# Optimization experiments

Measured on AMD Instinct MI355X. Metric: run time of the kernel, lower is better.

Reference implementation:

```python
import jax, jax.numpy as jnp
import numpy as np
import math

TAU = 1.0  # init kwarg tau


def setup_inputs() -> dict:
    key = jax.random.key(0)
    n, m = 1024, 8192
    V = jax.random.normal(key, (n, m), dtype=jnp.float32)
    return {"V": V}


def reference(V) -> jnp.ndarray:
    n, m = V.shape
    num_rounds = math.ceil(m / n)
    # Repeat V row-blocks num_rounds times: M has shape [num_rounds*n, m]
    M = jnp.tile(V, (num_rounds, 1))

    def step(c, row):
        # Soft round-robin pick (training branch of SoftRR.__one_round)
        y = jax.nn.softmax((row - jnp.min(row) + 1.0) * c / TAU)
        c = (1.0 - y) * c
        return c, y

    c0 = jnp.ones((m,), dtype=V.dtype)
    _, R = jax.lax.scan(step, c0, M)  # R: [num_rounds*n, m]
    pi = R.reshape(num_rounds, n, m).sum(axis=0)  # [n, m]
    return pi
```

## Files before the change

kernel.cpp:

```cpp
#include <hip/hip_runtime.h>
#include <hip/hip_fp16.h>


#define N_ROWS 1024
#define M_COLS 8192
#define STEPS  8192
#define LOG2E  1.4426950408889634f

using half8  = __attribute__((ext_vector_type(8))) _Float16;
using half2v = __attribute__((ext_vector_type(2))) _Float16;

__device__ __forceinline__ float fast_exp2(float x) {
#if __has_builtin(__builtin_amdgcn_exp2f)
  return __builtin_amdgcn_exp2f(x);
#else
  return exp2f(x);
#endif
}
__device__ __forceinline__ float fast_rcp(float x) {
#if __has_builtin(__builtin_amdgcn_rcpf)
  return __builtin_amdgcn_rcpf(x);
#else
  return 1.0f / x;
#endif
}
__device__ __forceinline__ half2v pack_f16(float y0, float y1) {
  return __builtin_bit_cast(half2v, __builtin_amdgcn_cvt_pkrtz(y0, y1));
}

template <int CTRL>
__device__ __forceinline__ float dpp_add(float x) {
  int yi = __builtin_amdgcn_update_dpp(0, __builtin_bit_cast(int, x),
                                       CTRL, 0xf, 0xf, true);
  return x + __builtin_bit_cast(float, yi);
}

__device__ __forceinline__ float wave_sum_to_lane63(float x) {
  x = dpp_add<0x111>(x);
  x = dpp_add<0x112>(x);
  x = dpp_add<0x114>(x);
  x = dpp_add<0x118>(x);
  x = dpp_add<0x142>(x);
  x = dpp_add<0x143>(x);
  return x;
}

#define BAR_LDS_ONLY() asm volatile("s_waitcnt lgkmcnt(0)\n\ts_barrier" ::: "memory")

__global__ void softrr_rowmin(const float* __restrict__ V, float* __restrict__ rmin) {
  const int row = blockIdx.x;
  const float* p = V + (size_t)row * M_COLS;
  float m = 1e30f;
  for (int j = threadIdx.x; j < M_COLS; j += 256) m = fminf(m, p[j]);
#pragma unroll
  for (int off = 32; off; off >>= 1) m = fminf(m, __shfl_xor(m, off, 64));
  __shared__ float sm[4];
  if ((threadIdx.x & 63) == 0) sm[threadIdx.x >> 6] = m;
  __syncthreads();
  if (threadIdx.x == 0) {
    rmin[row] = fminf(fminf(sm[0], sm[1]), fminf(sm[2], sm[3]));
  }
}

__global__ void softrr_prep(const float* __restrict__ V, const float* __restrict__ rmin,
                            __half* __restrict__ A) {
  const int idx8 = blockIdx.x * 256 + threadIdx.x;
  const int row = idx8 >> 10;
  const float mn = rmin[row];
  const float4* v4 = (const float4*)V;
  float4 va = v4[2 * idx8];
  float4 vb = v4[2 * idx8 + 1];
  half8 o;
  o[0] = (_Float16)((va.x - mn + 1.0f) * LOG2E);
  o[1] = (_Float16)((va.y - mn + 1.0f) * LOG2E);
  o[2] = (_Float16)((va.z - mn + 1.0f) * LOG2E);
  o[3] = (_Float16)((va.w - mn + 1.0f) * LOG2E);
  o[4] = (_Float16)((vb.x - mn + 1.0f) * LOG2E);
  o[5] = (_Float16)((vb.y - mn + 1.0f) * LOG2E);
  o[6] = (_Float16)((vb.z - mn + 1.0f) * LOG2E);
  o[7] = (_Float16)((vb.w - mn + 1.0f) * LOG2E);
  ((half8*)A)[idx8] = o;
}

__global__ void __launch_bounds__(512) softrr_scan_nor(const __half* __restrict__ Ah,
                                                       __half* __restrict__ Rh) {
  const int t = threadIdx.x;
  const int wave = t >> 6;
  const int lane = t & 63;
  __shared__ float sP[2][8];

  const half8* __restrict__ A8 = (const half8*)Ah;
  half8* __restrict__ R8 = (half8*)Rh;

  float c[16];
#pragma unroll
  for (int k = 0; k < 16; ++k) c[k] = 1.0f;

  half8 a_cur0 = A8[2 * t];
  half8 a_cur1 = A8[2 * t + 1];
  half8 a_nx0  = A8[1024 + 2 * t];
  half8 a_nx1  = A8[1024 + 2 * t + 1];

  for (int s = 0; s < STEPS; ++s) {
    const int ld  = (s + 2) & (N_ROWS - 1);
    const int par = s & 1;

    half8 an0 = A8[ld * 1024 + 2 * t];
    half8 an1 = A8[ld * 1024 + 2 * t + 1];

    float e[16];
#pragma unroll
    for (int k = 0; k < 8; ++k) {
      e[k]     = fast_exp2((float)a_cur0[k] * c[k]);
      e[8 + k] = fast_exp2((float)a_cur1[k] * c[8 + k]);
    }
    float l = (((e[0] + e[1]) + (e[2] + e[3])) + ((e[4] + e[5]) + (e[6] + e[7])))
            + (((e[8] + e[9]) + (e[10] + e[11])) + ((e[12] + e[13]) + (e[14] + e[15])));

    l = wave_sum_to_lane63(l);
    if (lane == 63) sP[par][wave] = l;
    BAR_LDS_ONLY();

    float x = (lane < 8) ? sP[par][lane] : 0.0f;
    x = dpp_add<0x111>(x);
    x = dpp_add<0x112>(x);
    x = dpp_add<0x114>(x);
    const float S = __builtin_bit_cast(
        float, __builtin_amdgcn_readlane(__builtin_bit_cast(int, x), 7));
    const float Sinv = fast_rcp(S);

    half8 o0, o1;
#pragma unroll
    for (int k = 0; k < 8; k += 2) {
      float y0 = e[k] * Sinv;
      float y1 = e[k + 1] * Sinv;
      c[k]     = __builtin_fmaf(-y0, c[k], c[k]);
      c[k + 1] = __builtin_fmaf(-y1, c[k + 1], c[k + 1]);
      half2v h = pack_f16(y0, y1);
      o0[k] = h[0]; o0[k + 1] = h[1];
    }
#pragma unroll
    for (int k = 0; k < 8; k += 2) {
      float y0 = e[8 + k] * Sinv;
      float y1 = e[8 + k + 1] * Sinv;
      c[8 + k]     = __builtin_fmaf(-y0, c[8 + k], c[8 + k]);
      c[8 + k + 1] = __builtin_fmaf(-y1, c[8 + k + 1], c[8 + k + 1]);
      half2v h = pack_f16(y0, y1);
      o1[k] = h[0]; o1[k + 1] = h[1];
    }
    R8[(size_t)s * 1024 + 2 * t]     = o0;
    R8[(size_t)s * 1024 + 2 * t + 1] = o1;

    a_cur0 = a_nx0; a_cur1 = a_nx1;
    a_nx0 = an0;    a_nx1 = an1;
  }
}

__global__ void softrr_sum8(const __half* __restrict__ Rh, float* __restrict__ out) {
  const int idx8 = blockIdx.x * 256 + threadIdx.x;
  const half8* R8 = (const half8*)Rh;
  float acc[8];
  {
    half8 v = R8[idx8];
#pragma unroll
    for (int k = 0; k < 8; ++k) acc[k] = (float)v[k];
  }
#pragma unroll
  for (int r = 1; r < 8; ++r) {
    half8 v = R8[(size_t)r * 1024 * 1024 + idx8];
#pragma unroll
    for (int k = 0; k < 8; ++k) acc[k] += (float)v[k];
  }
  ((float4*)out)[2 * idx8]     = make_float4(acc[0], acc[1], acc[2], acc[3]);
  ((float4*)out)[2 * idx8 + 1] = make_float4(acc[4], acc[5], acc[6], acc[7]);
}

__global__ void __launch_bounds__(512) softrr_scan_a(const __half* __restrict__ Ah,
                                                     __half* __restrict__ PIh) {
  const int t = threadIdx.x;
  const int wave = t >> 6;
  const int lane = t & 63;
  __shared__ float sP[2][8];
  const half8* __restrict__ A8 = (const half8*)Ah;
  half8* __restrict__ P8 = (half8*)PIh;
  float c[16];
#pragma unroll
  for (int k = 0; k < 16; ++k) c[k] = 1.0f;
  half8 a0 = A8[2 * t];
  half8 a1 = A8[2 * t + 1];
  half8 p0, p1;
  for (int s = 0; s < STEPS; ++s) {
    const int i = s & (N_ROWS - 1);
    const int r = s >> 10;
    const int in_ = (s + 1) & (N_ROWS - 1);
    const int par = s & 1;
    half8 an0 = A8[in_ * 1024 + 2 * t];
    half8 an1 = A8[in_ * 1024 + 2 * t + 1];
    float e[16];
#pragma unroll
    for (int k = 0; k < 8; ++k) {
      e[k]     = fast_exp2((float)a0[k] * c[k]);
      e[8 + k] = fast_exp2((float)a1[k] * c[8 + k]);
    }
    float l = (((e[0] + e[1]) + (e[2] + e[3])) + ((e[4] + e[5]) + (e[6] + e[7])))
            + (((e[8] + e[9]) + (e[10] + e[11])) + ((e[12] + e[13]) + (e[14] + e[15])));
    l = wave_sum_to_lane63(l);
    if (lane == 63) sP[par][wave] = l;
    BAR_LDS_ONLY();
    float x = (lane < 8) ? sP[par][lane] : 0.0f;
    x = dpp_add<0x111>(x);
    x = dpp_add<0x112>(x);
    x = dpp_add<0x114>(x);
    const float S = __builtin_bit_cast(
        float, __builtin_amdgcn_readlane(__builtin_bit_cast(int, x), 7));
    const float Sinv = fast_rcp(S);
    half8 o0, o1;
#pragma unroll
    for (int k = 0; k < 8; k += 2) {
      float y0 = e[k] * Sinv, y1 = e[k + 1] * Sinv;
      c[k] = __builtin_fmaf(-y0, c[k], c[k]);
      c[k + 1] = __builtin_fmaf(-y1, c[k + 1], c[k + 1]);
      half2v h = pack_f16(y0, y1);
      o0[k] = h[0]; o0[k + 1] = h[1];
    }
#pragma unroll
    for (int k = 0; k < 8; k += 2) {
      float y0 = e[8 + k] * Sinv, y1 = e[8 + k + 1] * Sinv;
      c[8 + k] = __builtin_fmaf(-y0, c[8 + k], c[8 + k]);
      c[8 + k + 1] = __builtin_fmaf(-y1, c[8 + k + 1], c[8 + k + 1]);
      half2v h = pack_f16(y0, y1);
      o1[k] = h[0]; o1[k + 1] = h[1];
    }
    if (r > 0) { o0 = o0 + p0; o1 = o1 + p1; }
    P8[i * 1024 + 2 * t]     = o0;
    P8[i * 1024 + 2 * t + 1] = o1;
    a0 = an0; a1 = an1;
    p0 = P8[in_ * 1024 + 2 * t];
    p1 = P8[in_ * 1024 + 2 * t + 1];
  }
}

__global__ void softrr_cvt(const __half* __restrict__ PIh, float* __restrict__ out) {
  const int idx8 = blockIdx.x * 256 + threadIdx.x;
  half8 p = ((const half8*)PIh)[idx8];
  ((float4*)out)[2 * idx8]     = make_float4((float)p[0], (float)p[1], (float)p[2], (float)p[3]);
  ((float4*)out)[2 * idx8 + 1] = make_float4((float)p[4], (float)p[5], (float)p[6], (float)p[7]);
}

__global__ void __launch_bounds__(1024) softrr_scan_b(const float* __restrict__ V,
                                                      const float* __restrict__ rmin,
                                                      float* __restrict__ out) {
  const int t = threadIdx.x;
  const int wave = t >> 6;
  const int lane = t & 63;
  __shared__ float partials[2][16];
  __shared__ float smin[N_ROWS];
  smin[t] = rmin[t];
  __syncthreads();
  const float4* __restrict__ V4 = (const float4*)V;
  float4* O4 = (float4*)out;
  float c[8];
#pragma unroll
  for (int k = 0; k < 8; ++k) c[k] = 1.0f;
  float4 va = V4[2 * t], vb = V4[2 * t + 1];
  float4 pa, pb;
  for (int s = 0; s < STEPS; ++s) {
    const int i = s & (N_ROWS - 1);
    const int r = s >> 10;
    const int in_ = (s + 1) & (N_ROWS - 1);
    float4 van = V4[in_ * 2048 + 2 * t];
    float4 vbn = V4[in_ * 2048 + 2 * t + 1];
    const float mn = smin[i];
    const float base = (1.0f - mn) * LOG2E;
    float vv[8] = {va.x, va.y, va.z, va.w, vb.x, vb.y, vb.z, vb.w};
    float e[8];
    float l = 0.0f;
#pragma unroll
    for (int k = 0; k < 8; ++k) {
      float zb = __builtin_fmaf(vv[k], LOG2E, base);
      e[k] = fast_exp2(zb * c[k]);
      l += e[k];
    }
#pragma unroll
    for (int off = 32; off; off >>= 1) l += __shfl_xor(l, off, 64);
    if (lane == 0) partials[s & 1][wave] = l;
    __syncthreads();
    float S = 0.0f;
#pragma unroll
    for (int w = 0; w < 16; ++w) S += partials[s & 1][w];
    const float Sinv = fast_rcp(S);
    float po[8] = {pa.x, pa.y, pa.z, pa.w, pb.x, pb.y, pb.z, pb.w};
    float o[8];
#pragma unroll
    for (int k = 0; k < 8; ++k) {
      float y = e[k] * Sinv;
      c[k] = __builtin_fmaf(-y, c[k], c[k]);
      o[k] = (r > 0) ? (po[k] + y) : y;
    }
    O4[i * 2048 + 2 * t]     = make_float4(o[0], o[1], o[2], o[3]);
    O4[i * 2048 + 2 * t + 1] = make_float4(o[4], o[5], o[6], o[7]);
    va = van; vb = vbn;
    pa = O4[in_ * 2048 + 2 * t];
    pb = O4[in_ * 2048 + 2 * t + 1];
  }
}

extern "C" void kernel_launch(void* const* d_in, const int* in_sizes, int n_in,
                              void* d_out, int out_size, void* d_ws, size_t ws_size,
                              hipStream_t stream) {
  const float* V = (const float*)d_in[0];
  float* out = (float*)d_out;
  float* rmin = (float*)d_ws;

  const size_t A_BYTES = (size_t)N_ROWS * M_COLS * 2;
  const size_t R_BYTES = (size_t)STEPS * M_COLS * 2;
  const size_t need_nor = 4096 + A_BYTES + R_BYTES;
  const size_t need_rmw = 4096 + A_BYTES + A_BYTES;

  if (ws_size >= need_nor) {
    __half* A = (__half*)((char*)d_ws + 4096);
    __half* R = (__half*)((char*)d_ws + 4096 + A_BYTES);
    softrr_rowmin<<<N_ROWS, 256, 0, stream>>>(V, rmin);
    softrr_prep<<<4096, 256, 0, stream>>>(V, rmin, A);
    softrr_scan_nor<<<1, 512, 0, stream>>>(A, R);
    softrr_sum8<<<4096, 256, 0, stream>>>(R, out);
  } else if (ws_size >= need_rmw) {
    __half* A  = (__half*)((char*)d_ws + 4096);
    __half* PI = (__half*)((char*)d_ws + 4096 + A_BYTES);
    softrr_rowmin<<<N_ROWS, 256, 0, stream>>>(V, rmin);
    softrr_prep<<<4096, 256, 0, stream>>>(V, rmin, A);
    softrr_scan_a<<<1, 512, 0, stream>>>(A, PI);
    softrr_cvt<<<4096, 256, 0, stream>>>(PI, out);
  } else {
    softrr_rowmin<<<N_ROWS, 256, 0, stream>>>(V, rmin);
    softrr_scan_b<<<1, 1024, 0, stream>>>(V, rmin, out);
  }
}
```

Before: 4.958 ms.

## Software-pipeline the softmax scan so output writes overlap the block reduction

Restructures the serial scan loop so each step deferred-writes the previous step's normalized output, computes the next step's exponentials and partial sums before the barrier, and needs only one barrier per step with the reduction read moved after it. The loop is unrolled by four with register rotation for a three-row-deep prefetch of the input rows. The intent is to shorten the critical path between barriers and hide global stores and loads behind the reduction latency. The cost is higher register pressure, and a prologue and epilogue must handle the first exponentials and the final row.

```diff
diff --git a/kernel.cpp b/kernel.cpp
--- a/kernel.cpp
+++ b/kernel.cpp
@@ -82,6 +82,64 @@
   ((half8*)A)[idx8] = o;
 }
 
+__device__ __forceinline__ void rr_step(
+    int s,
+    const half8& ac0, const half8& ac1, half8& ad0, half8& ad1,
+    float (&e)[16], float (&eo)[16], float (&c)[16], float& Sinv_prev,
+    const half8* __restrict__ A8, half8* __restrict__ R8,
+    float (*sP)[8], int t, int lane, int wave)
+{
+  const int par = s & 1;
+  float x = (lane < 8) ? sP[par][lane] : 0.0f;
+
+  half8 o0, o1;
+#pragma unroll
+  for (int k = 0; k < 8; k += 2) {
+    half2v h = pack_f16(eo[k] * Sinv_prev, eo[k + 1] * Sinv_prev);
+    o0[k] = h[0]; o0[k + 1] = h[1];
+  }
+#pragma unroll
+  for (int k = 0; k < 8; k += 2) {
+    half2v h = pack_f16(eo[8 + k] * Sinv_prev, eo[8 + k + 1] * Sinv_prev);
+    o1[k] = h[0]; o1[k + 1] = h[1];
+  }
+  const size_t rrow = (size_t)((s - 1) & (STEPS - 1));
+  R8[rrow * 1024 + 2 * t]     = o0;
+  R8[rrow * 1024 + 2 * t + 1] = o1;
+
+  float tt[16];
+#pragma unroll
+  for (int k = 0; k < 16; ++k) tt[k] = c[k] * e[k];
+
+  const int ld = (s + 3) & (N_ROWS - 1);
+  ad0 = A8[ld * 1024 + 2 * t];
+  ad1 = A8[ld * 1024 + 2 * t + 1];
+
+  x = dpp_add<0x111>(x);
+  x = dpp_add<0x112>(x);
+  x = dpp_add<0x114>(x);
+  const float S = __builtin_bit_cast(
+      float, __builtin_amdgcn_readlane(__builtin_bit_cast(int, x), 7));
+  const float Sinv = fast_rcp(S);
+
+#pragma unroll
+  for (int k = 0; k < 8; ++k) {
+    c[k] = __builtin_fmaf(-tt[k], Sinv, c[k]);
+    eo[k] = fast_exp2(__builtin_fmaf((float)ac0[k], c[k], 0.0f));
+  }
+#pragma unroll
+  for (int k = 0; k < 8; ++k) {
+    c[8 + k] = __builtin_fmaf(-tt[8 + k], Sinv, c[8 + k]);
+    eo[8 + k] = fast_exp2(__builtin_fmaf((float)ac1[k], c[8 + k], 0.0f));
+  }
+  float l = (((eo[0] + eo[1]) + (eo[2] + eo[3])) + ((eo[4] + eo[5]) + (eo[6] + eo[7])))
+          + (((eo[8] + eo[9]) + (eo[10] + eo[11])) + ((eo[12] + eo[13]) + (eo[14] + eo[15])));
+  l = wave_sum_to_lane63(l);
+  if (lane == 63) sP[par ^ 1][wave] = l;
+  Sinv_prev = Sinv;
+  BAR_LDS_ONLY();
+}
+
 __global__ void __launch_bounds__(512) softrr_scan_nor(const __half* __restrict__ Ah,
                                                        __half* __restrict__ Rh) {
   const int t = threadIdx.x;
@@ -92,67 +150,50 @@
   const half8* __restrict__ A8 = (const half8*)Ah;
   half8* __restrict__ R8 = (half8*)Rh;
 
-  float c[16];
-#pragma unroll
-  for (int k = 0; k < 16; ++k) c[k] = 1.0f;
-
-  half8 a_cur0 = A8[2 * t];
-  half8 a_cur1 = A8[2 * t + 1];
-  half8 a_nx0  = A8[1024 + 2 * t];
-  half8 a_nx1  = A8[1024 + 2 * t + 1];
-
-  for (int s = 0; s < STEPS; ++s) {
-    const int ld  = (s + 2) & (N_ROWS - 1);
-    const int par = s & 1;
-
-    half8 an0 = A8[ld * 1024 + 2 * t];
-    half8 an1 = A8[ld * 1024 + 2 * t + 1];
-
-    float e[16];
-#pragma unroll
-    for (int k = 0; k < 8; ++k) {
-      e[k]     = fast_exp2((float)a_cur0[k] * c[k]);
-      e[8 + k] = fast_exp2((float)a_cur1[k] * c[8 + k]);
-    }
-    float l = (((e[0] + e[1]) + (e[2] + e[3])) + ((e[4] + e[5]) + (e[6] + e[7])))
-            + (((e[8] + e[9]) + (e[10] + e[11])) + ((e[12] + e[13]) + (e[14] + e[15])));
-
+  float c[16], eX[16], eY[16];
+#pragma unroll
+  for (int k = 0; k < 16; ++k) { c[k] = 1.0f; eY[k] = 0.0f; }
+
+  half8 r0a = A8[2 * t], r0b = A8[2 * t + 1];
+  half8 pA0 = A8[1024 + 2 * t], pA1 = A8[1024 + 2 * t + 1];
+  half8 pB0 = A8[2048 + 2 * t], pB1 = A8[2048 + 2 * t + 1];
+  half8 pC0, pC1, pD0, pD1;
+
+#pragma unroll
+  for (int k = 0; k < 8; ++k) {
+    eX[k]     = fast_exp2((float)r0a[k]);
+    eX[8 + k] = fast_exp2((float)r0b[k]);
+  }
+  {
+    float l = (((eX[0] + eX[1]) + (eX[2] + eX[3])) + ((eX[4] + eX[5]) + (eX[6] + eX[7])))
+            + (((eX[8] + eX[9]) + (eX[10] + eX[11])) + ((eX[12] + eX[13]) + (eX[14] + eX[15])));
     l = wave_sum_to_lane63(l);
-    if (lane == 63) sP[par][wave] = l;
-    BAR_LDS_ONLY();
-
-    float x = (lane < 8) ? sP[par][lane] : 0.0f;
-    x = dpp_add<0x111>(x);
-    x = dpp_add<0x112>(x);
-    x = dpp_add<0x114>(x);
-    const float S = __builtin_bit_cast(
-        float, __builtin_amdgcn_readlane(__builtin_bit_cast(int, x), 7));
-    const float Sinv = fast_rcp(S);
-
+    if (lane == 63) sP[0][wave] = l;
+  }
+  float Sinv_prev = 0.0f;
+  BAR_LDS_ONLY();
+
+  for (int s = 0; s < STEPS; s += 4) {
+    rr_step(s + 0, pA0, pA1, pC0, pC1, eX, eY, c, Sinv_prev, A8, R8, sP, t, lane, wave);
+    rr_step(s + 1, pB0, pB1, pD0, pD1, eY, eX, c, Sinv_prev, A8, R8, sP, t, lane, wave);
+    rr_step(s + 2, pC0, pC1, pA0, pA1, eX, eY, c, Sinv_prev, A8, R8, sP, t, lane, wave);
+    rr_step(s + 3, pD0, pD1, pB0, pB1, eY, eX, c, Sinv_prev, A8, R8, sP, t, lane, wave);
+  }
+
+  {
     half8 o0, o1;
 #pragma unroll
     for (int k = 0; k < 8; k += 2) {
-      float y0 = e[k] * Sinv;
-      float y1 = e[k + 1] * Sinv;
-      c[k]     = __builtin_fmaf(-y0, c[k], c[k]);
-      c[k + 1] = __builtin_fmaf(-y1, c[k + 1], c[k + 1]);
-      half2v h = pack_f16(y0, y1);
+      half2v h = pack_f16(eY[k] * Sinv_prev, eY[k + 1] * Sinv_prev);
       o0[k] = h[0]; o0[k + 1] = h[1];
     }
 #pragma unroll
     for (int k = 0; k < 8; k += 2) {
-      float y0 = e[8 + k] * Sinv;
-      float y1 = e[8 + k + 1] * Sinv;
-      c[8 + k]     = __builtin_fmaf(-y0, c[8 + k], c[8 + k]);
-      c[8 + k + 1] = __builtin_fmaf(-y1, c[8 + k + 1], c[8 + k + 1]);
-      half2v h = pack_f16(y0, y1);
+      half2v h = pack_f16(eY[8 + k] * Sinv_prev, eY[8 + k + 1] * Sinv_prev);
       o1[k] = h[0]; o1[k + 1] = h[1];
     }
-    R8[(size_t)s * 1024 + 2 * t]     = o0;
-    R8[(size_t)s * 1024 + 2 * t + 1] = o1;
-
-    a_cur0 = a_nx0; a_cur1 = a_nx1;
-    a_nx0 = an0;    a_nx1 = an1;
+    R8[(size_t)(STEPS - 1) * 1024 + 2 * t]     = o0;
+    R8[(size_t)(STEPS - 1) * 1024 + 2 * t + 1] = o1;
   }
 }
 
```

Measured after the change: 4.972 ms. About the same (+0.3%).

## Double threads per step and software-pipeline the softmax scan across steps

Applied to the files above, without the earlier changes.

Doubles the scan block to 1024 threads so each thread owns 8 columns instead of 16, which halves the per-thread serial work per step. The step is reordered so that the next step's exponentials and wave partial sums are computed right after the current normaliser is known. This leaves one barrier per step, and the output store is deferred by one step. Loads prefetch three rows ahead, rotating through four registers in a 4-way unrolled loop. The cost is a larger 16-wave cross-wave reduction with one more DPP stage, and more waves synchronising at each barrier.

```diff
diff --git a/kernel.cpp b/kernel.cpp
--- a/kernel.cpp
+++ b/kernel.cpp
@@ -82,78 +82,92 @@
   ((half8*)A)[idx8] = o;
 }
 
-__global__ void __launch_bounds__(512) softrr_scan_nor(const __half* __restrict__ Ah,
-                                                       __half* __restrict__ Rh) {
+__device__ __forceinline__ void rr_step(
+    int s,
+    const half8& acur, half8& adst,
+    float (&e)[8], float (&c)[8], half8& o,
+    const half8* __restrict__ A8, half8* __restrict__ R8,
+    float (*sP)[16], int t, int lane, int wave)
+{
+  const int par = s & 1;
+  float x = (lane < 16) ? sP[par][lane] : 0.0f;
+
+  R8[(size_t)((s - 1) & (STEPS - 1)) * 1024 + t] = o;
+
+  adst = A8[((s + 3) & (N_ROWS - 1)) * 1024 + t];
+
+  x = dpp_add<0x111>(x);
+  x = dpp_add<0x112>(x);
+  x = dpp_add<0x114>(x);
+  x = dpp_add<0x118>(x);
+  const float S = __builtin_bit_cast(
+      float, __builtin_amdgcn_readlane(__builtin_bit_cast(int, x), 15));
+  const float Sinv = fast_rcp(S);
+
+  float y[8];
+#pragma unroll
+  for (int k = 0; k < 8; ++k) {
+    y[k] = e[k] * Sinv;
+    c[k] = __builtin_fmaf(-y[k], c[k], c[k]);
+    e[k] = fast_exp2(__builtin_fmaf((float)acur[k], c[k], 0.0f));
+  }
+  float l = ((e[0] + e[1]) + (e[2] + e[3])) + ((e[4] + e[5]) + (e[6] + e[7]));
+  l = wave_sum_to_lane63(l);
+  if (lane == 63) sP[par ^ 1][wave] = l;
+
+  {
+    half2v h0 = pack_f16(y[0], y[1]);
+    half2v h1 = pack_f16(y[2], y[3]);
+    half2v h2 = pack_f16(y[4], y[5]);
+    half2v h3 = pack_f16(y[6], y[7]);
+    o[0] = h0[0]; o[1] = h0[1]; o[2] = h1[0]; o[3] = h1[1];
+    o[4] = h2[0]; o[5] = h2[1]; o[6] = h3[0]; o[7] = h3[1];
+  }
+  BAR_LDS_ONLY();
+}
+
+__global__ void __launch_bounds__(1024) softrr_scan_nor(const __half* __restrict__ Ah,
+                                                        __half* __restrict__ Rh) {
   const int t = threadIdx.x;
   const int wave = t >> 6;
   const int lane = t & 63;
-  __shared__ float sP[2][8];
+  __shared__ float sP[2][16];
 
   const half8* __restrict__ A8 = (const half8*)Ah;
   half8* __restrict__ R8 = (half8*)Rh;
 
-  float c[16];
-#pragma unroll
-  for (int k = 0; k < 16; ++k) c[k] = 1.0f;
-
-  half8 a_cur0 = A8[2 * t];
-  half8 a_cur1 = A8[2 * t + 1];
-  half8 a_nx0  = A8[1024 + 2 * t];
-  half8 a_nx1  = A8[1024 + 2 * t + 1];
-
-  for (int s = 0; s < STEPS; ++s) {
-    const int ld  = (s + 2) & (N_ROWS - 1);
-    const int par = s & 1;
-
-    half8 an0 = A8[ld * 1024 + 2 * t];
-    half8 an1 = A8[ld * 1024 + 2 * t + 1];
-
-    float e[16];
-#pragma unroll
-    for (int k = 0; k < 8; ++k) {
-      e[k]     = fast_exp2((float)a_cur0[k] * c[k]);
-      e[8 + k] = fast_exp2((float)a_cur1[k] * c[8 + k]);
-    }
-    float l = (((e[0] + e[1]) + (e[2] + e[3])) + ((e[4] + e[5]) + (e[6] + e[7])))
-            + (((e[8] + e[9]) + (e[10] + e[11])) + ((e[12] + e[13]) + (e[14] + e[15])));
-
+  float c[8], e[8];
+#pragma unroll
+  for (int k = 0; k < 8; ++k) c[k] = 1.0f;
+
+  half8 r0 = A8[t];
+  half8 pA = A8[1024 + t];
+  half8 pB = A8[2048 + t];
+  half8 pC, pD;
+
+#pragma unroll
+  for (int k = 0; k < 8; ++k) e[k] = fast_exp2((float)r0[k]);
+  {
+    float l = ((e[0] + e[1]) + (e[2] + e[3])) + ((e[4] + e[5]) + (e[6] + e[7]));
     l = wave_sum_to_lane63(l);
-    if (lane == 63) sP[par][wave] = l;
-    BAR_LDS_ONLY();
-
-    float x = (lane < 8) ? sP[par][lane] : 0.0f;
-    x = dpp_add<0x111>(x);
-    x = dpp_add<0x112>(x);
-    x = dpp_add<0x114>(x);
-    const float S = __builtin_bit_cast(
-        float, __builtin_amdgcn_readlane(__builtin_bit_cast(int, x), 7));
-    const float Sinv = fast_rcp(S);
-
-    half8 o0, o1;
-#pragma unroll
-    for (int k = 0; k < 8; k += 2) {
-      float y0 = e[k] * Sinv;
-      float y1 = e[k + 1] * Sinv;
-      c[k]     = __builtin_fmaf(-y0, c[k], c[k]);
-      c[k + 1] = __builtin_fmaf(-y1, c[k + 1], c[k + 1]);
-      half2v h = pack_f16(y0, y1);
-      o0[k] = h[0]; o0[k + 1] = h[1];
-    }
-#pragma unroll
-    for (int k = 0; k < 8; k += 2) {
-      float y0 = e[8 + k] * Sinv;
-      float y1 = e[8 + k + 1] * Sinv;
-      c[8 + k]     = __builtin_fmaf(-y0, c[8 + k], c[8 + k]);
-      c[8 + k + 1] = __builtin_fmaf(-y1, c[8 + k + 1], c[8 + k + 1]);
-      half2v h = pack_f16(y0, y1);
-      o1[k] = h[0]; o1[k + 1] = h[1];
-    }
-    R8[(size_t)s * 1024 + 2 * t]     = o0;
-    R8[(size_t)s * 1024 + 2 * t + 1] = o1;
-
-    a_cur0 = a_nx0; a_cur1 = a_nx1;
-    a_nx0 = an0;    a_nx1 = an1;
-  }
+    if (lane == 63) sP[0][wave] = l;
+  }
+  half8 o;
+  {
+    half2v z = pack_f16(0.0f, 0.0f);
+    o[0]=z[0]; o[1]=z[1]; o[2]=z[0]; o[3]=z[1];
+    o[4]=z[0]; o[5]=z[1]; o[6]=z[0]; o[7]=z[1];
+  }
+  BAR_LDS_ONLY();
+
+  for (int s = 0; s < STEPS; s += 4) {
+    rr_step(s + 0, pA, pC, e, c, o, A8, R8, sP, t, lane, wave);
+    rr_step(s + 1, pB, pD, e, c, o, A8, R8, sP, t, lane, wave);
+    rr_step(s + 2, pC, pA, e, c, o, A8, R8, sP, t, lane, wave);
+    rr_step(s + 3, pD, pB, e, c, o, A8, R8, sP, t, lane, wave);
+  }
+
+  R8[(size_t)(STEPS - 1) * 1024 + t] = o;
 }
 
 __global__ void softrr_sum8(const __half* __restrict__ Rh, float* __restrict__ out) {
@@ -322,7 +336,7 @@
     __half* R = (__half*)((char*)d_ws + 4096 + A_BYTES);
     softrr_rowmin<<<N_ROWS, 256, 0, stream>>>(V, rmin);
     softrr_prep<<<4096, 256, 0, stream>>>(V, rmin, A);
-    softrr_scan_nor<<<1, 512, 0, stream>>>(A, R);
+    softrr_scan_nor<<<1, 1024, 0, stream>>>(A, R);
     softrr_sum8<<<4096, 256, 0, stream>>>(R, out);
   } else if (ws_size >= need_rmw) {
     __half* A  = (__half*)((char*)d_ws + 4096);
```

Measured after the change: 4.288 ms. 1.16x faster.
